# Performance work log

Measured on AMD Instinct MI355X. Metric: run time of the kernel, lower is better.

Reference implementation:

```python
import jax, jax.numpy as jnp
import numpy as np

N_NODES = 50000

def _add_self_loops(edge_index, n):
    loop = jnp.arange(n, dtype=edge_index.dtype)
    src = jnp.concatenate([edge_index[0], loop])
    dst = jnp.concatenate([edge_index[1], loop])
    return src, dst

def _gcn_conv(x, src, dst, W, b, n):
    h = x @ W
    deg = jax.ops.segment_sum(jnp.ones_like(dst, dtype=h.dtype), dst, num_segments=n)
    inv_sqrt = jnp.where(deg > 0, jax.lax.rsqrt(deg), 0.0)
    coef = inv_sqrt[src] * inv_sqrt[dst]            # [E]
    msg = h[src] * coef[:, None]                     # [E, hidden]
    return jax.ops.segment_sum(msg, dst, num_segments=n) + b

def _gat_conv(x, src, dst, W, att_src, att_dst, b, n, heads, out_dim):
    # PyG GATConv, concat=False -> mean over heads; self-loops already added
    h = (x @ W).reshape(n, heads, out_dim)           # [N, H, F]
    a_src = jnp.sum(h * att_src, axis=-1)            # [N, H]
    a_dst = jnp.sum(h * att_dst, axis=-1)            # [N, H]
    e = a_src[src] + a_dst[dst]                      # [E, H]
    e = jax.nn.leaky_relu(e, negative_slope=0.2)
    # neighborhood softmax over edges grouped by destination
    m = jax.ops.segment_max(e, dst, num_segments=n)  # [N, H]
    ex = jnp.exp(e - m[dst])
    denom = jax.ops.segment_sum(ex, dst, num_segments=n)
    alpha = ex / denom[dst]                          # [E, H]
    out = jax.ops.segment_sum(h[src] * alpha[:, :, None], dst, num_segments=n)  # [N, H, F]
    return out.mean(axis=1) + b                      # concat=False -> head mean

def setup_inputs() -> dict:
    key = jax.random.key(0)
    ks = jax.random.split(key, 12)
    n, input_dim, hidden, output_dim, heads = N_NODES, 128, 128, 64, 2
    gat_out = hidden // 2
    x = jax.random.normal(ks[0], (n, input_dim), dtype=jnp.float32)
    edge_index = jax.random.randint(ks[1], (2, 800000), 0, n, dtype=jnp.int64)
    s = lambda fi, fo: float(np.sqrt(1.0 / fi))
    W1 = jax.random.normal(ks[2], (input_dim, hidden), dtype=jnp.float32) * s(input_dim, hidden)
    b1 = jnp.zeros((hidden,), dtype=jnp.float32)
    Wg = jax.random.normal(ks[3], (hidden, heads * gat_out), dtype=jnp.float32) * s(hidden, gat_out)
    att_src = jax.random.normal(ks[4], (heads, gat_out), dtype=jnp.float32) * s(gat_out, 1)
    att_dst = jax.random.normal(ks[5], (heads, gat_out), dtype=jnp.float32) * s(gat_out, 1)
    bg = jnp.zeros((gat_out,), dtype=jnp.float32)
    W3 = jax.random.normal(ks[6], (gat_out, output_dim), dtype=jnp.float32) * s(gat_out, output_dim)
    b3 = jnp.zeros((output_dim,), dtype=jnp.float32)
    return {"x": x, "edge_index": edge_index, "W1": W1, "b1": b1, "Wg": Wg,
            "att_src": att_src, "att_dst": att_dst, "bg": bg, "W3": W3, "b3": b3}

def reference(x, edge_index, W1, b1, Wg, att_src, att_dst, bg, W3, b3):
    n = x.shape[0]
    heads, gat_out = att_src.shape
    src, dst = _add_self_loops(edge_index, n)
    # dropout is identity in eval mode
    h = _gcn_conv(x, src, dst, W1, b1, n)
    h = jax.nn.relu(h)
    h = _gat_conv(h, src, dst, Wg, att_src, att_dst, bg, n, heads, gat_out)
    h = jax.nn.elu(h)
    return _gcn_conv(h, src, dst, W3, b3, n)
```

## Files before the change

### kernel.cpp

```cpp
#include <hip/hip_runtime.h>
#include <hip/hip_bf16.h>
#include <math.h>

#define N_NODES 50000
#define E0      800000
#define E_TOT   (E0 + N_NODES)
#define SCAP    512

using bf16 = __hip_bfloat16;
typedef __attribute__((ext_vector_type(8))) short bfrag;
typedef __attribute__((ext_vector_type(4))) float ffrag;

static __device__ __forceinline__ float bfu2f_lo(unsigned u){ return __uint_as_float(u << 16); }
static __device__ __forceinline__ float bfu2f_hi(unsigned u){ return __uint_as_float(u & 0xffff0000u); }

static __device__ __forceinline__ unsigned packbf(float a, float b){
    bf16 x = __float2bfloat16(a), y = __float2bfloat16(b);
    unsigned short ux = *reinterpret_cast<unsigned short*>(&x);
    unsigned short uy = *reinterpret_cast<unsigned short*>(&y);
    return ((unsigned)uy << 16) | ux;
}

static __device__ __forceinline__ int detect_f32(const unsigned* xu){
    int lane = threadIdx.x & 63;
    unsigned ex = (xu[lane] >> 7) & 0xFF;
    return (__ballot(ex < 100 || ex > 140) != 0ULL);
}
static __device__ __forceinline__ int detect_i32(const int* ei){
    int lane = threadIdx.x & 63;
    return (__ballot(ei[2 * lane + 1] != 0) != 0ULL);
}

static __device__ __forceinline__ float ldany(const void* p, int i, int isf32){
    return isf32 ? ((const float*)p)[i] : __bfloat162float(((const bf16*)p)[i]);
}

__global__ void k_convert(const void* __restrict__ xv,
                          const void* W1, const void* Wg, const void* W3,
                          const void* b1, const void* bg, const void* b3,
                          const void* as_, const void* ad_,
                          bf16* __restrict__ W1p, bf16* __restrict__ Wgp,
                          bf16* __restrict__ W3p, float* __restrict__ vecf,
                          bf16* __restrict__ xb, int* __restrict__ deg){
    const int NXB = (N_NODES * 128 + 255) / 256;
    int b = blockIdx.x, t = threadIdx.x;
    if (b >= 148 + NXB){
        int i = (b - 148 - NXB) * 256 + t;
        if (i < N_NODES) deg[i] = 0;
        return;
    }
    int isf = detect_f32((const unsigned*)xv);
    if (b >= 148){
        int i = (b - 148) * 256 + t;
        if (i < N_NODES * 128) xb[i] = __float2bfloat16(ldany(xv, i, isf));
        return;
    }
    if (b < 16){
        int dd = b * 256 + t;
        int j  = dd & 7;
        int L  = (dd >> 3) & 63;
        int kc = (dd >> 9) & 1;
        int ct = dd >> 10;
        int k = kc * 32 + ((L >> 4) << 3) + j;
        int n = ct * 16 + (L & 15);
        W3p[dd] = __float2bfloat16(ldany(W3, k * 64 + n, isf));
    }
    else if (b < 18){
        int i = (b - 16) * 256 + t;
        float v;
        if      (i < 128) v = ldany(b1,  i,       isf);
        else if (i < 192) v = ldany(bg,  i - 128, isf);
        else if (i < 256) v = ldany(b3,  i - 192, isf);
        else if (i < 384) v = ldany(as_, i - 256, isf);
        else              v = ldany(ad_, i - 384, isf);
        vecf[i] = v;
    } else {
        int d = (b - 18) * 256 + t;
        const void* Wsrc = (d < 16384) ? W1 : Wg;
        bf16* Wdst = (d < 16384) ? W1p : Wgp;
        int dd = d & 16383;
        int j  = dd & 7;
        int L  = (dd >> 3) & 63;
        int kc = (dd >> 9) & 3;
        int ct = dd >> 11;
        int k = kc * 32 + ((L >> 4) << 3) + j;
        int n = ct * 16 + (L & 15);
        Wdst[dd] = __float2bfloat16(ldany(Wsrc, k * 128 + n, isf));
    }
}


static __device__ __forceinline__ int load_dst(const int* ei, int e, int is32){
    if (e >= E0) return e - E0;
    return is32 ? ei[E0 + e] : (int)((const long long*)ei)[E0 + e];
}
static __device__ __forceinline__ int load_src(const int* ei, int e, int is32){
    if (e >= E0) return e - E0;
    return is32 ? ei[e] : (int)((const long long*)ei)[e];
}

__global__ void k_count(const int* __restrict__ ei, int* __restrict__ deg,
                        int* __restrict__ rank){
    int is32 = detect_i32(ei);
    int e = blockIdx.x * blockDim.x + threadIdx.x;
    if (e >= E_TOT) return;
    int dst = load_dst(ei, e, is32);
    int src = load_src(ei, e, is32);
    if ((unsigned)dst >= N_NODES || (unsigned)src >= N_NODES) return;
    rank[e] = atomicAdd(&deg[dst], 1);
}

__global__ void k_scanA(const int* __restrict__ deg, int* __restrict__ tmp, int* __restrict__ blk){
    __shared__ int s[256];
    int t = threadIdx.x;
    int i = blockIdx.x * 256 + t;
    int v = (i < N_NODES) ? deg[i] : 0;
    s[t] = v; __syncthreads();
    for (int off = 1; off < 256; off <<= 1){
        int x = (t >= off) ? s[t - off] : 0;
        __syncthreads();
        s[t] += x;
        __syncthreads();
    }
    if (t == 255) blk[blockIdx.x] = s[255];
    if (i < N_NODES) tmp[i] = s[t] - v;
}

__global__ void k_scanB(int* __restrict__ blk, int nb){
    __shared__ int s[256];
    int t = threadIdx.x;
    int v = (t < nb) ? blk[t] : 0;
    s[t] = v; __syncthreads();
    for (int off = 1; off < 256; off <<= 1){
        int x = (t >= off) ? s[t - off] : 0;
        __syncthreads();
        s[t] += x;
        __syncthreads();
    }
    if (t < nb) blk[t] = s[t] - v;
}

__global__ void k_scanC(int* __restrict__ row_ptr, const int* __restrict__ blk,
                        const int* __restrict__ deg, float* __restrict__ inv_sqrt){
    int i = blockIdx.x * blockDim.x + threadIdx.x;
    if (i < N_NODES){
        row_ptr[i] += blk[i >> 8];
        int d = deg[i];
        inv_sqrt[i] = (d > 0) ? rsqrtf((float)d) : 0.0f;
    }
    if (i == 0) row_ptr[N_NODES] = E_TOT;
}

__global__ void k_fill(const int* __restrict__ ei, const int* __restrict__ row_ptr,
                       const float* __restrict__ isq, const int* __restrict__ rank,
                       int2* __restrict__ ecr){
    int is32 = detect_i32(ei);
    int e = blockIdx.x * blockDim.x + threadIdx.x;
    if (e >= E_TOT) return;
    int dst = load_dst(ei, e, is32);
    int src = load_src(ei, e, is32);
    if ((unsigned)dst >= N_NODES || (unsigned)src >= N_NODES) return;
    int pos = row_ptr[dst] + rank[e];
    float c = isq[dst] * isq[src];
    ecr[pos] = make_int2(src, __float_as_int(c));
}

__global__ __launch_bounds__(256, 2) void k_gather(
        const ushort2* __restrict__ xb2, const int* __restrict__ rp,
        const int2* __restrict__ ecr, unsigned* __restrict__ Xa){
    __shared__ int   scsr[SCAP];
    __shared__ float scf[SCAP];
    int n0 = blockIdx.x * 4;
    int b0 = rp[n0];
    int tot  = rp[n0 + 4] - b0;
    int stot = min(tot, SCAP);
    for (int i = threadIdx.x; i < stot; i += 256){
        int2 ev = ecr[b0 + i];
        scsr[i] = ev.x;
        scf[i]  = __int_as_float(ev.y);
    }
    __syncthreads();

    int w = threadIdx.x >> 6, l = threadIdx.x & 63;
    int n = n0 + w;
    float a0 = 0.f, a1 = 0.f;
    int b = rp[n] - b0, e = rp[n + 1] - b0;
    int elim = min(e, stot);
    #pragma unroll 4
    for (int i = b; i < elim; ++i){
        int s = scsr[i];
        float c = scf[i];
        ushort2 v = xb2[(size_t)s * 64 + l];
        a0 += c * __uint_as_float((unsigned)v.x << 16);
        a1 += c * __uint_as_float((unsigned)v.y << 16);
    }
    for (int i = max(b, stot); i < e; ++i){
        int2 ev = ecr[b0 + i];
        float c = __int_as_float(ev.y);
        ushort2 v = xb2[(size_t)ev.x * 64 + l];
        a0 += c * __uint_as_float((unsigned)v.x << 16);
        a1 += c * __uint_as_float((unsigned)v.y << 16);
    }
    Xa[(size_t)n * 64 + l] = packbf(a0, a1);
}

template<int EPI>
__global__ __launch_bounds__(512) void k_gemm_mfma(
        const bf16* __restrict__ A, const bf16* __restrict__ Wp,
        const float* __restrict__ vecf, bf16* __restrict__ O){
    int wid  = threadIdx.x >> 6;
    int lane = threadIdx.x & 63;
    int n0 = blockIdx.x * 16;
    int m = lane & 15, q = lane >> 4;

    const bfrag* Ap = (const bfrag*)(A + (size_t)(n0 + m) * 128);
    const bfrag* Bp = (const bfrag*)Wp + (size_t)wid * 256 + lane;

    ffrag c = {0.f, 0.f, 0.f, 0.f};
    #pragma unroll
    for (int kc = 0; kc < 4; ++kc){
        bfrag af = Ap[kc * 4 + q];
        bfrag bf = Bp[kc * 64];
        c = __builtin_amdgcn_mfma_f32_16x16x32_bf16(af, bf, c, 0, 0, 0);
    }
    __syncthreads();

    int col = wid * 16 + m;
    if (EPI == 0){
        float bb = vecf[col];
        #pragma unroll
        for (int r = 0; r < 4; ++r){
            int row = n0 + q * 4 + r;
            O[(size_t)row * 128 + col] = __float2bfloat16(fmaxf(c[r] + bb, 0.f));
        }
    } else {
        int f = col & 63, h = col >> 6;
        #pragma unroll
        for (int r = 0; r < 4; ++r){
            int row = n0 + q * 4 + r;
            O[(size_t)row * 128 + f * 2 + h] = __float2bfloat16(c[r]);
        }
    }
}

__global__ __launch_bounds__(256) void k_gemm_z(
        const bf16* __restrict__ Y, const bf16* __restrict__ W3p,
        bf16* __restrict__ Z){
    int wid  = threadIdx.x >> 6;
    int lane = threadIdx.x & 63;
    int n0 = blockIdx.x * 16;
    int m = lane & 15, q = lane >> 4;

    const bfrag* Ap = (const bfrag*)(Y + (size_t)(n0 + m) * 64);
    const bfrag* Bp = (const bfrag*)W3p + (size_t)wid * 128 + lane;

    ffrag c = {0.f, 0.f, 0.f, 0.f};
    #pragma unroll
    for (int kc = 0; kc < 2; ++kc){
        bfrag af = Ap[kc * 4 + q];
        bfrag bf = Bp[kc * 64];
        c = __builtin_amdgcn_mfma_f32_16x16x32_bf16(af, bf, c, 0, 0, 0);
    }
    int col = wid * 16 + m;
    #pragma unroll
    for (int r = 0; r < 4; ++r){
        int row = n0 + q * 4 + r;
        Z[(size_t)row * 64 + col] = __float2bfloat16(c[r]);
    }
}

__global__ __launch_bounds__(256) void k_att(
        const unsigned* __restrict__ X2u, const float* __restrict__ vecf,
        float2* __restrict__ a_src, float2* __restrict__ a_dst){
    int n = blockIdx.x * 4 + (threadIdx.x >> 6);
    int l = threadIdx.x & 63;
    unsigned v = X2u[(size_t)n * 64 + l];
    float x0 = bfu2f_lo(v), x1 = bfu2f_hi(v);
    float s0 = x0 * vecf[256 + l], s1 = x1 * vecf[320 + l];
    float d0 = x0 * vecf[384 + l], d1 = x1 * vecf[448 + l];
    for (int off = 32; off; off >>= 1){
        s0 += __shfl_down(s0, off, 64);  s1 += __shfl_down(s1, off, 64);
        d0 += __shfl_down(d0, off, 64);  d1 += __shfl_down(d1, off, 64);
    }
    if (l == 0){
        a_src[n] = make_float2(s0, s1);
        a_dst[n] = make_float2(d0, d1);
    }
}

__global__ __launch_bounds__(256) void k_gat(
        const unsigned* __restrict__ X2u, const int* __restrict__ rp,
        const int2* __restrict__ ecr, const float2* __restrict__ a_src,
        const float2* __restrict__ a_dst, const float* __restrict__ vecf,
        bf16* __restrict__ Y){
    __shared__ int    scsr[SCAP];
    __shared__ float2 pe[SCAP];
    int n0 = blockIdx.x * 4;
    int b0 = rp[n0];
    int tot  = rp[n0 + 4] - b0;
    int stot = min(tot, SCAP);
    for (int i = threadIdx.x; i < stot; i += 256) scsr[i] = ecr[b0 + i].x;
    __syncthreads();

    int w = threadIdx.x >> 6, f = threadIdx.x & 63;
    int n = n0 + w;
    float2 ad = a_dst[n];
    int b = rp[n] - b0, e = rp[n + 1] - b0;
    int elim = min(e, stot);

    for (int i = b + f; i < elim; i += 64){
        float2 av = a_src[scsr[i]];
        float e0 = av.x + ad.x, e1 = av.y + ad.y;
        e0 = (e0 > 0.f) ? e0 : 0.2f * e0;
        e1 = (e1 > 0.f) ? e1 : 0.2f * e1;
        pe[i] = make_float2(__expf(e0), __expf(e1));
    }

    float l0 = 0.f, l1 = 0.f, o0 = 0.f, o1 = 0.f;
    #pragma unroll 4
    for (int i = b; i < elim; ++i){
        float2 p = pe[i];
        unsigned v = X2u[(size_t)scsr[i] * 64 + f];
        l0 += p.x;  o0 += p.x * bfu2f_lo(v);
        l1 += p.y;  o1 += p.y * bfu2f_hi(v);
    }
    for (int i = max(b, stot); i < e; ++i){
        int s = ecr[b0 + i].x;
        float2 av = a_src[s];
        unsigned v = X2u[(size_t)s * 64 + f];
        float e0 = av.x + ad.x, e1 = av.y + ad.y;
        e0 = (e0 > 0.f) ? e0 : 0.2f * e0;
        e1 = (e1 > 0.f) ? e1 : 0.2f * e1;
        float p0 = __expf(e0), p1 = __expf(e1);
        l0 += p0;  o0 += p0 * bfu2f_lo(v);
        l1 += p1;  o1 += p1 * bfu2f_hi(v);
    }
    float val = 0.5f * (o0 / l0 + o1 / l1) + vecf[128 + f];
    val = (val > 0.f) ? val : expm1f(val);
    Y[(size_t)n * 64 + f] = __float2bfloat16(val);
}

__global__ __launch_bounds__(256) void k_gather_out(
        const bf16* __restrict__ Z, const int* __restrict__ rp,
        const int2* __restrict__ ecr, const float* __restrict__ vecf,
        float* __restrict__ out){
    __shared__ int   scsr[SCAP];
    __shared__ float scf[SCAP];
    int n0 = blockIdx.x * 4;
    int b0 = rp[n0];
    int tot  = rp[n0 + 4] - b0;
    int stot = min(tot, SCAP);
    for (int i = threadIdx.x; i < stot; i += 256){
        int2 ev = ecr[b0 + i];
        scsr[i] = ev.x;
        scf[i]  = __int_as_float(ev.y);
    }
    __syncthreads();

    int w = threadIdx.x >> 6, f = threadIdx.x & 63;
    int n = n0 + w;
    float a = vecf[192 + f];
    int b = rp[n] - b0, e = rp[n + 1] - b0;
    int elim = min(e, stot);
    #pragma unroll 4
    for (int i = b; i < elim; ++i)
        a += scf[i] * __bfloat162float(Z[(size_t)scsr[i] * 64 + f]);
    for (int i = max(b, stot); i < e; ++i){
        int2 ev = ecr[b0 + i];
        a += __int_as_float(ev.y) * __bfloat162float(Z[(size_t)ev.x * 64 + f]);
    }
    out[(size_t)n * 64 + f] = a;
}


extern "C" void kernel_launch(void* const* d_in, const int* in_sizes, int n_in,
                              void* d_out, int out_size, void* d_ws, size_t ws_size,
                              hipStream_t stream) {
    const void* x  = d_in[0];
    const int*  ei = (const int*)d_in[1];
    float* out = (float*)d_out;

    char* p = (char*)d_ws;
    auto alloc = [&](size_t bytes) -> void* {
        void* r = (void*)p;
        p += (bytes + 255) & ~(size_t)255;
        return r;
    };
    int*   deg      = (int*)  alloc((size_t)N_NODES * 4);
    int*   row_ptr  = (int*)  alloc((size_t)(N_NODES + 1) * 4);
    int*   blk      = (int*)  alloc(256 * 4);
    int*   rank     = (int*)  alloc((size_t)E_TOT * 4);
    int2*  ecr      = (int2*) alloc((size_t)E_TOT * 8);
    float* inv_sqrt = (float*)alloc((size_t)N_NODES * 4);
    float* a_src    = (float*)alloc((size_t)N_NODES * 2 * 4);
    float* a_dst    = (float*)alloc((size_t)N_NODES * 2 * 4);
    bf16*  W1p      = (bf16*) alloc(16384 * 2);
    bf16*  Wgp      = (bf16*) alloc(16384 * 2);
    bf16*  W3p      = (bf16*) alloc(4096 * 2);
    float* vecf     = (float*)alloc(512 * 4);
    bf16*  xb       = (bf16*) alloc((size_t)N_NODES * 128 * 2);
    bf16*  XA       = (bf16*) alloc((size_t)N_NODES * 128 * 2);
    bf16*  Y        = (bf16*) alloc((size_t)N_NODES * 64 * 2);
    bf16*  Z        = xb;

    const int NB_NODE = (N_NODES + 255) / 256;
    const int NB_EDGE = (E_TOT + 255) / 256;
    const int NXB     = (N_NODES * 128 + 255) / 256;
    const int NB_CONV = 148 + NXB + NB_NODE;

    k_convert<<<NB_CONV, 256, 0, stream>>>(x, d_in[2], d_in[4], d_in[8],
                                           d_in[3], d_in[7], d_in[9], d_in[5], d_in[6],
                                           W1p, Wgp, W3p, vecf, xb, deg);
    k_count<<<NB_EDGE, 256, 0, stream>>>(ei, deg, rank);
    k_scanA<<<NB_NODE, 256, 0, stream>>>(deg, row_ptr, blk);
    k_scanB<<<1, 256, 0, stream>>>(blk, NB_NODE);
    k_scanC<<<NB_NODE, 256, 0, stream>>>(row_ptr, blk, deg, inv_sqrt);
    k_fill<<<NB_EDGE, 256, 0, stream>>>(ei, row_ptr, inv_sqrt, rank, ecr);

    k_gather<<<N_NODES / 4, 256, 0, stream>>>((const ushort2*)xb, row_ptr, ecr,
                                              (unsigned*)XA);
    k_gemm_mfma<0><<<N_NODES / 16, 512, 0, stream>>>(XA, W1p, vecf, XA);
    k_gemm_mfma<1><<<N_NODES / 16, 512, 0, stream>>>(XA, Wgp, vecf, XA);
    k_att<<<N_NODES / 4, 256, 0, stream>>>((const unsigned*)XA, vecf, (float2*)a_src, (float2*)a_dst);
    k_gat<<<N_NODES / 4, 256, 0, stream>>>((const unsigned*)XA, row_ptr, ecr,
                                           (const float2*)a_src, (const float2*)a_dst,
                                           vecf, Y);
    k_gemm_z<<<N_NODES / 16, 256, 0, stream>>>(Y, W3p, Z);
    k_gather_out<<<N_NODES / 4, 256, 0, stream>>>(Z, row_ptr, ecr, vecf, out);
}
```

Before: 311.9 us.

## Fuse attention scores into GAT GEMM, merge scan kernels, split gathers across half-waves

The attention-coefficient kernel is folded into the GAT projection GEMM epilogue, which reduces the per-row dot products through shuffles and shared memory. The separate block-sum scan kernel is dropped, and each scanC block now reduces its own prefix of block sums. The three gather kernels now have each half-wave process alternate edges with wider vector loads, then combine the halves with a cross-lane shuffle. This doubles memory-level parallelism per node and cuts launches, at the cost of extra shuffles and redundant block-sum work.

```diff
diff --git a/kernel.cpp b/kernel.cpp
--- a/kernel.cpp
+++ b/kernel.cpp
@@ -13,6 +13,7 @@
 
 static __device__ __forceinline__ float bfu2f_lo(unsigned u){ return __uint_as_float(u << 16); }
 static __device__ __forceinline__ float bfu2f_hi(unsigned u){ return __uint_as_float(u & 0xffff0000u); }
+static __device__ __forceinline__ float us2f(unsigned short u){ return __uint_as_float((unsigned)u << 16); }
 
 static __device__ __forceinline__ unsigned packbf(float a, float b){
     bf16 x = __float2bfloat16(a), y = __float2bfloat16(b);
@@ -126,25 +127,22 @@
     if (i < N_NODES) tmp[i] = s[t] - v;
 }
 
-__global__ void k_scanB(int* __restrict__ blk, int nb){
+__global__ void k_scanC(int* __restrict__ row_ptr, const int* __restrict__ blk,
+                        const int* __restrict__ deg, float* __restrict__ inv_sqrt,
+                        int nb){
     __shared__ int s[256];
     int t = threadIdx.x;
-    int v = (t < nb) ? blk[t] : 0;
-    s[t] = v; __syncthreads();
-    for (int off = 1; off < 256; off <<= 1){
-        int x = (t >= off) ? s[t - off] : 0;
+    int B = blockIdx.x;
+    s[t] = (t < nb && t < B) ? blk[t] : 0;
+    __syncthreads();
+    for (int off = 128; off; off >>= 1){
+        if (t < off) s[t] += s[t + off];
         __syncthreads();
-        s[t] += x;
-        __syncthreads();
-    }
-    if (t < nb) blk[t] = s[t] - v;
-}
-
-__global__ void k_scanC(int* __restrict__ row_ptr, const int* __restrict__ blk,
-                        const int* __restrict__ deg, float* __restrict__ inv_sqrt){
-    int i = blockIdx.x * blockDim.x + threadIdx.x;
+    }
+    int base = s[0];
+    int i = B * 256 + t;
     if (i < N_NODES){
-        row_ptr[i] += blk[i >> 8];
+        row_ptr[i] += base;
         int d = deg[i];
         inv_sqrt[i] = (d > 0) ? rsqrtf((float)d) : 0.0f;
     }
@@ -166,8 +164,8 @@
 }
 
 __global__ __launch_bounds__(256, 2) void k_gather(
-        const ushort2* __restrict__ xb2, const int* __restrict__ rp,
-        const int2* __restrict__ ecr, unsigned* __restrict__ Xa){
+        const ushort4* __restrict__ xb4, const int* __restrict__ rp,
+        const int2* __restrict__ ecr, uint2* __restrict__ Xa){
     __shared__ int   scsr[SCAP];
     __shared__ float scf[SCAP];
     int n0 = blockIdx.x * 4;
@@ -181,33 +179,43 @@
     }
     __syncthreads();
 
-    int w = threadIdx.x >> 6, l = threadIdx.x & 63;
+    int w    = threadIdx.x >> 6;
+    int half = (threadIdx.x >> 5) & 1;
+    int fz   = threadIdx.x & 31;
     int n = n0 + w;
-    float a0 = 0.f, a1 = 0.f;
+    float a0 = 0.f, a1 = 0.f, a2 = 0.f, a3 = 0.f;
     int b = rp[n] - b0, e = rp[n + 1] - b0;
     int elim = min(e, stot);
     #pragma unroll 4
-    for (int i = b; i < elim; ++i){
+    for (int i = b + half; i < elim; i += 2){
         int s = scsr[i];
         float c = scf[i];
-        ushort2 v = xb2[(size_t)s * 64 + l];
-        a0 += c * __uint_as_float((unsigned)v.x << 16);
-        a1 += c * __uint_as_float((unsigned)v.y << 16);
-    }
-    for (int i = max(b, stot); i < e; ++i){
+        ushort4 v = xb4[(size_t)s * 32 + fz];
+        a0 += c * us2f(v.x);  a1 += c * us2f(v.y);
+        a2 += c * us2f(v.z);  a3 += c * us2f(v.w);
+    }
+    int start = max(b, stot);
+    int i0 = start + (((b + half) ^ start) & 1);
+    for (int i = i0; i < e; i += 2){
         int2 ev = ecr[b0 + i];
         float c = __int_as_float(ev.y);
-        ushort2 v = xb2[(size_t)ev.x * 64 + l];
-        a0 += c * __uint_as_float((unsigned)v.x << 16);
-        a1 += c * __uint_as_float((unsigned)v.y << 16);
-    }
-    Xa[(size_t)n * 64 + l] = packbf(a0, a1);
+        ushort4 v = xb4[(size_t)ev.x * 32 + fz];
+        a0 += c * us2f(v.x);  a1 += c * us2f(v.y);
+        a2 += c * us2f(v.z);  a3 += c * us2f(v.w);
+    }
+    a0 += __shfl_xor(a0, 32, 64);  a1 += __shfl_xor(a1, 32, 64);
+    a2 += __shfl_xor(a2, 32, 64);  a3 += __shfl_xor(a3, 32, 64);
+    if (half == 0)
+        Xa[(size_t)n * 32 + fz] = make_uint2(packbf(a0, a1), packbf(a2, a3));
 }
 
 template<int EPI>
 __global__ __launch_bounds__(512) void k_gemm_mfma(
         const bf16* __restrict__ A, const bf16* __restrict__ Wp,
-        const float* __restrict__ vecf, bf16* __restrict__ O){
+        const float* __restrict__ vecf, bf16* __restrict__ O,
+        float* __restrict__ aS, float* __restrict__ aD){
+    __shared__ float sA[16][8];
+    __shared__ float sD[16][8];
     int wid  = threadIdx.x >> 6;
     int lane = threadIdx.x & 63;
     int n0 = blockIdx.x * 16;
@@ -235,10 +243,41 @@
         }
     } else {
         int f = col & 63, h = col >> 6;
+        float as_v = vecf[256 + h * 64 + f];
+        float ad_v = vecf[384 + h * 64 + f];
+        float ps[4], pd[4];
         #pragma unroll
         for (int r = 0; r < 4; ++r){
             int row = n0 + q * 4 + r;
             O[(size_t)row * 128 + f * 2 + h] = __float2bfloat16(c[r]);
+            ps[r] = c[r] * as_v;
+            pd[r] = c[r] * ad_v;
+        }
+        #pragma unroll
+        for (int off = 1; off < 16; off <<= 1){
+            #pragma unroll
+            for (int r = 0; r < 4; ++r){
+                ps[r] += __shfl_xor(ps[r], off, 64);
+                pd[r] += __shfl_xor(pd[r], off, 64);
+            }
+        }
+        if (m == 0){
+            #pragma unroll
+            for (int r = 0; r < 4; ++r){
+                int rl = q * 4 + r;
+                sA[rl][wid] = ps[r];
+                sD[rl][wid] = pd[r];
+            }
+        }
+        __syncthreads();
+        int t = threadIdx.x;
+        if (t < 64){
+            int rl = t >> 2, hh = (t >> 1) & 1, which = t & 1;
+            const float (*S)[8] = which ? sD : sA;
+            float v = S[rl][hh * 4 + 0] + S[rl][hh * 4 + 1]
+                    + S[rl][hh * 4 + 2] + S[rl][hh * 4 + 3];
+            float* dp = which ? aD : aS;
+            dp[(size_t)(n0 + rl) * 2 + hh] = v;
         }
     }
 }
@@ -269,30 +308,11 @@
     }
 }
 
-__global__ __launch_bounds__(256) void k_att(
-        const unsigned* __restrict__ X2u, const float* __restrict__ vecf,
-        float2* __restrict__ a_src, float2* __restrict__ a_dst){
-    int n = blockIdx.x * 4 + (threadIdx.x >> 6);
-    int l = threadIdx.x & 63;
-    unsigned v = X2u[(size_t)n * 64 + l];
-    float x0 = bfu2f_lo(v), x1 = bfu2f_hi(v);
-    float s0 = x0 * vecf[256 + l], s1 = x1 * vecf[320 + l];
-    float d0 = x0 * vecf[384 + l], d1 = x1 * vecf[448 + l];
-    for (int off = 32; off; off >>= 1){
-        s0 += __shfl_down(s0, off, 64);  s1 += __shfl_down(s1, off, 64);
-        d0 += __shfl_down(d0, off, 64);  d1 += __shfl_down(d1, off, 64);
-    }
-    if (l == 0){
-        a_src[n] = make_float2(s0, s1);
-        a_dst[n] = make_float2(d0, d1);
-    }
-}
-
 __global__ __launch_bounds__(256) void k_gat(
-        const unsigned* __restrict__ X2u, const int* __restrict__ rp,
+        const uint2* __restrict__ X2u2, const int* __restrict__ rp,
         const int2* __restrict__ ecr, const float2* __restrict__ a_src,
         const float2* __restrict__ a_dst, const float* __restrict__ vecf,
-        bf16* __restrict__ Y){
+        unsigned* __restrict__ Yu){
     __shared__ int    scsr[SCAP];
     __shared__ float2 pe[SCAP];
     int n0 = blockIdx.x * 4;
@@ -302,7 +322,10 @@
     for (int i = threadIdx.x; i < stot; i += 256) scsr[i] = ecr[b0 + i].x;
     __syncthreads();
 
-    int w = threadIdx.x >> 6, f = threadIdx.x & 63;
+    int w    = threadIdx.x >> 6;
+    int f    = threadIdx.x & 63;
+    int half = (threadIdx.x >> 5) & 1;
+    int fz   = threadIdx.x & 31;
     int n = n0 + w;
     float2 ad = a_dst[n];
     int b = rp[n] - b0, e = rp[n + 1] - b0;
@@ -316,34 +339,46 @@
         pe[i] = make_float2(__expf(e0), __expf(e1));
     }
 
-    float l0 = 0.f, l1 = 0.f, o0 = 0.f, o1 = 0.f;
+    float l0 = 0.f, l1 = 0.f;
+    float o00 = 0.f, o01 = 0.f, o10 = 0.f, o11 = 0.f;
     #pragma unroll 4
-    for (int i = b; i < elim; ++i){
+    for (int i = b + half; i < elim; i += 2){
         float2 p = pe[i];
-        unsigned v = X2u[(size_t)scsr[i] * 64 + f];
-        l0 += p.x;  o0 += p.x * bfu2f_lo(v);
-        l1 += p.y;  o1 += p.y * bfu2f_hi(v);
-    }
-    for (int i = max(b, stot); i < e; ++i){
+        uint2 v = X2u2[(size_t)scsr[i] * 32 + fz];
+        l0  += p.x;                 l1  += p.y;
+        o00 += p.x * bfu2f_lo(v.x); o01 += p.y * bfu2f_hi(v.x);
+        o10 += p.x * bfu2f_lo(v.y); o11 += p.y * bfu2f_hi(v.y);
+    }
+    int start = max(b, stot);
+    int i0 = start + (((b + half) ^ start) & 1);
+    for (int i = i0; i < e; i += 2){
         int s = ecr[b0 + i].x;
         float2 av = a_src[s];
-        unsigned v = X2u[(size_t)s * 64 + f];
+        uint2 v = X2u2[(size_t)s * 32 + fz];
         float e0 = av.x + ad.x, e1 = av.y + ad.y;
         e0 = (e0 > 0.f) ? e0 : 0.2f * e0;
         e1 = (e1 > 0.f) ? e1 : 0.2f * e1;
         float p0 = __expf(e0), p1 = __expf(e1);
-        l0 += p0;  o0 += p0 * bfu2f_lo(v);
-        l1 += p1;  o1 += p1 * bfu2f_hi(v);
-    }
-    float val = 0.5f * (o0 / l0 + o1 / l1) + vecf[128 + f];
-    val = (val > 0.f) ? val : expm1f(val);
-    Y[(size_t)n * 64 + f] = __float2bfloat16(val);
+        l0  += p0;                 l1  += p1;
+        o00 += p0 * bfu2f_lo(v.x); o01 += p1 * bfu2f_hi(v.x);
+        o10 += p0 * bfu2f_lo(v.y); o11 += p1 * bfu2f_hi(v.y);
+    }
+    l0  += __shfl_xor(l0, 32, 64);   l1  += __shfl_xor(l1, 32, 64);
+    o00 += __shfl_xor(o00, 32, 64);  o01 += __shfl_xor(o01, 32, 64);
+    o10 += __shfl_xor(o10, 32, 64);  o11 += __shfl_xor(o11, 32, 64);
+    if (half == 0){
+        float v0 = 0.5f * (o00 / l0 + o01 / l1) + vecf[128 + 2 * fz];
+        float v1 = 0.5f * (o10 / l0 + o11 / l1) + vecf[128 + 2 * fz + 1];
+        v0 = (v0 > 0.f) ? v0 : expm1f(v0);
+        v1 = (v1 > 0.f) ? v1 : expm1f(v1);
+        Yu[(size_t)n * 32 + fz] = packbf(v0, v1);
+    }
 }
 
 __global__ __launch_bounds__(256) void k_gather_out(
-        const bf16* __restrict__ Z, const int* __restrict__ rp,
+        const unsigned* __restrict__ Zu, const int* __restrict__ rp,
         const int2* __restrict__ ecr, const float* __restrict__ vecf,
-        float* __restrict__ out){
+        float2* __restrict__ out2){
     __shared__ int   scsr[SCAP];
     __shared__ float scf[SCAP];
     int n0 = blockIdx.x * 4;
@@ -357,19 +392,34 @@
     }
     __syncthreads();
 
-    int w = threadIdx.x >> 6, f = threadIdx.x & 63;
+    int w    = threadIdx.x >> 6;
+    int half = (threadIdx.x >> 5) & 1;
+    int fz   = threadIdx.x & 31;
     int n = n0 + w;
-    float a = vecf[192 + f];
+    float a0 = 0.f, a1 = 0.f;
     int b = rp[n] - b0, e = rp[n + 1] - b0;
     int elim = min(e, stot);
     #pragma unroll 4
-    for (int i = b; i < elim; ++i)
-        a += scf[i] * __bfloat162float(Z[(size_t)scsr[i] * 64 + f]);
-    for (int i = max(b, stot); i < e; ++i){
+    for (int i = b + half; i < elim; i += 2){
+        float c = scf[i];
+        unsigned v = Zu[(size_t)scsr[i] * 32 + fz];
+        a0 += c * bfu2f_lo(v);
+        a1 += c * bfu2f_hi(v);
+    }
+    int start = max(b, stot);
+    int i0 = start + (((b + half) ^ start) & 1);
+    for (int i = i0; i < e; i += 2){
         int2 ev = ecr[b0 + i];
-        a += __int_as_float(ev.y) * __bfloat162float(Z[(size_t)ev.x * 64 + f]);
-    }
-    out[(size_t)n * 64 + f] = a;
+        float c = __int_as_float(ev.y);
+        unsigned v = Zu[(size_t)ev.x * 32 + fz];
+        a0 += c * bfu2f_lo(v);
+        a1 += c * bfu2f_hi(v);
+    }
+    a0 += __shfl_xor(a0, 32, 64);
+    a1 += __shfl_xor(a1, 32, 64);
+    if (half == 0)
+        out2[(size_t)n * 32 + fz] =
+            make_float2(a0 + vecf[192 + 2 * fz], a1 + vecf[192 + 2 * fz + 1]);
 }
 
 
@@ -413,18 +463,19 @@
                                            W1p, Wgp, W3p, vecf, xb, deg);
     k_count<<<NB_EDGE, 256, 0, stream>>>(ei, deg, rank);
     k_scanA<<<NB_NODE, 256, 0, stream>>>(deg, row_ptr, blk);
-    k_scanB<<<1, 256, 0, stream>>>(blk, NB_NODE);
-    k_scanC<<<NB_NODE, 256, 0, stream>>>(row_ptr, blk, deg, inv_sqrt);
+    k_scanC<<<NB_NODE, 256, 0, stream>>>(row_ptr, blk, deg, inv_sqrt, NB_NODE);
     k_fill<<<NB_EDGE, 256, 0, stream>>>(ei, row_ptr, inv_sqrt, rank, ecr);
 
-    k_gather<<<N_NODES / 4, 256, 0, stream>>>((const ushort2*)xb, row_ptr, ecr,
-                                              (unsigned*)XA);
-    k_gemm_mfma<0><<<N_NODES / 16, 512, 0, stream>>>(XA, W1p, vecf, XA);
-    k_gemm_mfma<1><<<N_NODES / 16, 512, 0, stream>>>(XA, Wgp, vecf, XA);
-    k_att<<<N_NODES / 4, 256, 0, stream>>>((const unsigned*)XA, vecf, (float2*)a_src, (float2*)a_dst);
-    k_gat<<<N_NODES / 4, 256, 0, stream>>>((const unsigned*)XA, row_ptr, ecr,
+    k_gather<<<N_NODES / 4, 256, 0, stream>>>((const ushort4*)xb, row_ptr, ecr,
+                                              (uint2*)XA);
+    k_gemm_mfma<0><<<N_NODES / 16, 512, 0, stream>>>(XA, W1p, vecf, XA,
+                                                     nullptr, nullptr);
+    k_gemm_mfma<1><<<N_NODES / 16, 512, 0, stream>>>(XA, Wgp, vecf, XA,
+                                                     a_src, a_dst);
+    k_gat<<<N_NODES / 4, 256, 0, stream>>>((const uint2*)XA, row_ptr, ecr,
                                            (const float2*)a_src, (const float2*)a_dst,
-                                           vecf, Y);
+                                           vecf, (unsigned*)Y);
     k_gemm_z<<<N_NODES / 16, 256, 0, stream>>>(Y, W3p, Z);
-    k_gather_out<<<N_NODES / 4, 256, 0, stream>>>(Z, row_ptr, ecr, vecf, out);
-}
+    k_gather_out<<<N_NODES / 4, 256, 0, stream>>>((const unsigned*)Z, row_ptr, ecr,
+                                                  vecf, (float2*)out);
+}
```

Result: faster. 289.9 us (-7.1%).
